# Kernel optimization log

Hardware: AMD Instinct MI355X
Metric: run time of the kernel (lower is better)

The kernel has to match this reference:

```python
import jax, jax.numpy as jnp
import numpy as np
from jax import lax

B, BERT_DIM, Z_DIM, ODE_UNITS, T_MAX = 4096, 768, 64, 128, 512
LN_EPS = 1e-5

def _glorot(key, shape):
    fan_in, fan_out = shape[0], shape[1]
    lim = float(np.sqrt(6.0 / (fan_in + fan_out)))
    return jax.random.uniform(key, shape, jnp.float32, -lim, lim)

def setup_inputs() -> dict:
    key = jax.random.key(0)
    ks = jax.random.split(key, 16)
    inp = {
        'bert_emb': jax.random.normal(ks[0], (B, BERT_DIM), jnp.float32),
        'times': jax.random.uniform(ks[1], (B, T_MAX), jnp.float32),
        'seq_lens': jax.random.randint(ks[2], (B,), 0, T_MAX).astype(jnp.int64),
        'eps': jax.random.normal(ks[3], (B, Z_DIM), jnp.float32),
        # bert_proj: Linear(768->64) + LayerNorm(64)
        'proj_W': _glorot(ks[4], (BERT_DIM, Z_DIM)),
        'proj_b': jnp.zeros((Z_DIM,), jnp.float32),
        'ln_g': jnp.ones((Z_DIM,), jnp.float32),
        'ln_b': jnp.zeros((Z_DIM,), jnp.float32),
        # DiffusionAug
        'log_noise_std': jnp.float32(-2.0),
        'den_W1': _glorot(ks[5], (Z_DIM, 2 * Z_DIM)),
        'den_b1': jnp.zeros((2 * Z_DIM,), jnp.float32),
        'den_W2': _glorot(ks[6], (2 * Z_DIM, Z_DIM)),
        'den_b2': jnp.zeros((Z_DIM,), jnp.float32),
        # ODEFunc: Linear->Tanh->Linear->Tanh->Linear (xavier_uniform, zero bias)
        'ode_W1': _glorot(ks[7], (Z_DIM, ODE_UNITS)),
        'ode_b1': jnp.zeros((ODE_UNITS,), jnp.float32),
        'ode_W2': _glorot(ks[8], (ODE_UNITS, ODE_UNITS)),
        'ode_b2': jnp.zeros((ODE_UNITS,), jnp.float32),
        'ode_W3': _glorot(ks[9], (ODE_UNITS, Z_DIM)),
        'ode_b3': jnp.zeros((Z_DIM,), jnp.float32),
        # dec_head: Linear(64->2)
        'dec_W': _glorot(ks[10], (Z_DIM, 2)),
        'dec_b': jnp.zeros((2,), jnp.float32),
    }
    return inp

def reference(bert_emb, times, seq_lens, eps, proj_W, proj_b, ln_g, ln_b,
              log_noise_std, den_W1, den_b1, den_W2, den_b2,
              ode_W1, ode_b1, ode_W2, ode_b2, ode_W3, ode_b3, dec_W, dec_b):
    T = times.shape[1]
    # bert_proj: Linear + LayerNorm (dropout = identity in eval)
    h = bert_emb @ proj_W + proj_b
    mu = jnp.mean(h, axis=-1, keepdims=True)
    var = jnp.var(h, axis=-1, keepdims=True)
    z_clean = (h - mu) * lax.rsqrt(var + LN_EPS) * ln_g + ln_b
    # DiffusionAug: noise + denoise MLP, MSE to detached clean latent
    sigma = jax.nn.softplus(log_noise_std)
    z_noisy = z_clean + sigma * eps
    z_aug = jax.nn.silu(z_noisy @ den_W1 + den_b1) @ den_W2 + den_b2
    diff_loss = jnp.mean((z_aug - lax.stop_gradient(z_clean)) ** 2)
    # Euler ODE integration: z <- z + dt * f(z), T sequential steps
    dt = jnp.float32(1.0 / max(T, 1))
    def step(z, _):
        f = jnp.tanh(jnp.tanh(z @ ode_W1 + ode_b1) @ ode_W2 + ode_b2) @ ode_W3 + ode_b3
        z_new = z + dt * f
        return z_new, z_new
    _, zs = lax.scan(step, z_aug, None, length=T)  # zs: (T, B, z)
    traj = jnp.concatenate([z_aug[:, None, :], jnp.swapaxes(zs, 0, 1)], axis=1)  # (B, T+1, z)
    out = traj @ dec_W + dec_b  # (B, T+1, 2)
    pred_delta = out[:, :, 0]
    stop_logits = out[:, :, 1]
    return (pred_delta, stop_logits, diff_loss)
```

## Files before the change

kernel.cpp:

```cpp
#include <hip/hip_runtime.h>
#include <stdint.h>

#define NB 4096
#define NT 512
#define OT 513
#define TOTE (NB*OT)
#define LOSSOFF (2*TOTE)

typedef float  f32x4 __attribute__((ext_vector_type(4)));
typedef __fp16 f16x8 __attribute__((ext_vector_type(8)));
typedef __fp16 f16x2 __attribute__((ext_vector_type(2)));

#define MFMA(A,B,C) __builtin_amdgcn_mfma_f32_16x16x32_f16((A),(B),(C),0,0,0)

__device__ __forceinline__ void wg_barrier() {
  asm volatile("s_waitcnt lgkmcnt(0)\n\ts_barrier" ::: "memory");
}

__device__ __forceinline__ float fast_tanh(float x) {
  float e = __builtin_amdgcn_exp2f(x * 2.8853900817779268f);
  return __builtin_fmaf(-2.0f, __builtin_amdgcn_rcpf(1.0f + e), 1.0f);
}
__device__ __forceinline__ f32x4 tanh4(f32x4 x) {
  f32x4 m = x * 2.8853900817779268f;
  f32x4 e;
  e.x = __builtin_amdgcn_exp2f(m.x); e.y = __builtin_amdgcn_exp2f(m.y);
  e.z = __builtin_amdgcn_exp2f(m.z); e.w = __builtin_amdgcn_exp2f(m.w);
  f32x4 o = e + 1.0f;
  f32x4 r;
  r.x = __builtin_amdgcn_rcpf(o.x); r.y = __builtin_amdgcn_rcpf(o.y);
  r.z = __builtin_amdgcn_rcpf(o.z); r.w = __builtin_amdgcn_rcpf(o.w);
  return __builtin_elementwise_fma((f32x4)(-2.0f), r, (f32x4)(1.0f));
}
__device__ __forceinline__ float fast_silu(float x) {
  float e = __builtin_amdgcn_exp2f(x * -1.4426950408889634f);
  return x * __builtin_amdgcn_rcpf(1.0f + e);
}
__device__ __forceinline__ uint32_t pk2(float a, float b) {
  union { f16x2 h; uint32_t u; } c;
  c.h = __builtin_amdgcn_cvt_pkrtz(a, b);
  return c.u;
}
__device__ __forceinline__ f16x8 pack8(f32x4 a, f32x4 b) {
  union { f16x8 v; f16x2 h[4]; } u;
  u.h[0] = __builtin_amdgcn_cvt_pkrtz(a.x, a.y);
  u.h[1] = __builtin_amdgcn_cvt_pkrtz(a.z, a.w);
  u.h[2] = __builtin_amdgcn_cvt_pkrtz(b.x, b.y);
  u.h[3] = __builtin_amdgcn_cvt_pkrtz(b.z, b.w);
  return u.v;
}

#define WS_WPAK (1u<<20)
#define WS_UBUF ((1u<<20) + (256u<<10))
#define WS_CBUF ((1u<<20) + (384u<<10))

__global__ void compose_kernel(const float* __restrict__ oW1, const float* __restrict__ oW3,
                               const float* __restrict__ ob3, const float* __restrict__ dW,
                               float* __restrict__ Ubuf, float* __restrict__ cbuf,
                               float* __restrict__ dout) {
  int g = blockIdx.x, tid = threadIdx.x;
  if (g < 72) {
    int e = g * 256 + tid;
    int i = e / 144, j = e - i * 144;
    float s = 0.f;
    if (j < 128) {
      #pragma unroll 4
      for (int k = 0; k < 64; k++) s = __builtin_fmaf(oW3[i * 64 + k], oW1[k * 128 + j], s);
    } else if (j < 130) {
      int cc = j - 128;
      for (int k = 0; k < 64; k++) s = __builtin_fmaf(oW3[i * 64 + k], dW[k * 2 + cc], s);
    }
    Ubuf[i * 144 + j] = s;
  } else {
    if (tid < 144) {
      float s = 0.f;
      if (tid < 128) {
        for (int k = 0; k < 64; k++) s = __builtin_fmaf(ob3[k], oW1[k * 128 + tid], s);
      } else if (tid < 130) {
        int cc = tid - 128;
        for (int k = 0; k < 64; k++) s = __builtin_fmaf(ob3[k], dW[k * 2 + cc], s);
      }
      cbuf[tid] = s;
    }
    if (tid == 255) dout[LOSSOFF] = 0.0f;
  }
}

__global__ void pack_kernel(const float* __restrict__ oW1, const float* __restrict__ oW2,
                            const float* __restrict__ dW,  const float* __restrict__ dW1,
                            const float* __restrict__ dW2, const float* __restrict__ pW,
                            const float* __restrict__ Ubuf, char* __restrict__ wdst) {
  int g = blockIdx.x * 256 + threadIdx.x;
  int fid = g >> 6, lane = g & 63;
  if (fid >= 228 || (fid >= 50 && fid < 64)) return;
  int m4 = lane & 15;
  if (fid >= 48 && fid < 50) {
    int kt = fid - 48;
    int k0 = kt * 32 + (lane >> 4) * 8;
    f16x8 out;
    #pragma unroll
    for (int j = 0; j < 8; j++) out[j] = (m4 < 2) ? (__fp16)dW[(k0 + j) * 2 + m4] : (__fp16)0.f;
    *(f16x8*)(wdst + (size_t)(fid * 64 + lane) * 16) = out;
    return;
  }
  const float* src; int Kt, M, base;
  if      (fid < 16)  { src = oW1;  Kt = 2;  M = 128; base = 0;   }
  else if (fid < 48)  { src = oW2;  Kt = 4;  M = 128; base = 16;  }
  else if (fid < 80)  { src = dW1;  Kt = 2;  M = 128; base = 64;  }
  else if (fid < 96)  { src = dW2;  Kt = 4;  M = 64;  base = 80;  }
  else if (fid < 192) { src = pW;   Kt = 24; M = 64;  base = 96;  }
  else                { src = Ubuf; Kt = 4;  M = 144; base = 192; }
  int local = fid - base;
  int mt = local / Kt, kt = local % Kt;
  int m  = mt * 16 + m4;
  int k0 = kt * 32 + (lane >> 4) * 8;
  f16x8 out;
  #pragma unroll
  for (int j = 0; j < 8; j++) out[j] = (__fp16)src[(size_t)(k0 + j) * M + m];
  *(f16x8*)(wdst + (size_t)(fid * 64 + lane) * 16) = out;
}

__global__ __launch_bounds__(512, 2) void prologue_kernel(
    const float* __restrict__ bert, const float* __restrict__ eps,
    const float* __restrict__ projb, const float* __restrict__ lng,
    const float* __restrict__ lnb,  const float* __restrict__ lns,
    const float* __restrict__ db1,  const float* __restrict__ db2,
    const char* __restrict__ wpack, float* __restrict__ wsz,
    float* __restrict__ dout) {
  __shared__ __attribute__((aligned(16))) char sZ[16 * 128];
  __shared__ __attribute__((aligned(16))) char sH[16 * 256];
  __shared__ f32x4  sScr[4 * 64];
  __shared__ float2 sMV[64];
  __shared__ float  sLsum[4];

  const int tid  = threadIdx.x;
  const int wave = tid >> 6, lane = tid & 63;
  const int q = lane >> 4, b = lane & 15;
  const int bg = blockIdx.x * 16 + b;
  const int b7 = b & 7;
  const f16x8* wp = (const f16x8*)wpack;
  const int u0 = wave * 16 + q * 4;

  const int zr0 = b * 128 + ((q    ) ^ b7) * 16;
  const int zr1 = b * 128 + ((q + 4) ^ b7) * 16;
  int hr[4];
  #pragma unroll
  for (int s = 0; s < 4; s++) hr[s] = b * 256 + ((4 * s + q) ^ b7) * 16;
  const int hw = b * 256 + (((2 * wave + (q >> 1)) ^ b7) * 16) + (q & 1) * 8;
  const int zw = b * 128 + (((2 * (wave & 3) + (q >> 1)) ^ b7) * 16) + (q & 1) * 8;

  const int mt = wave & 3, kh = wave >> 2;
  f32x4 hA = {0,0,0,0}, hB = {0,0,0,0};
  #pragma unroll 4
  for (int i = 0; i < 12; i++) {
    int kt = kh * 12 + i;
    f16x8 af = wp[(size_t)(96 + mt * 24 + kt) * 64 + lane];
    const float* bp = bert + (size_t)bg * 768 + kt * 32 + q * 8;
    f32x4 f0 = *(const f32x4*)bp;
    f32x4 f1 = *(const f32x4*)(bp + 4);
    f16x8 bf = pack8(f0, f1);
    if (i & 1) hB = MFMA(af, bf, hB); else hA = MFMA(af, bf, hA);
  }
  f32x4 hacc = hA + hB;
  if (wave >= 4) sScr[(wave - 4) * 64 + lane] = hacc;
  __syncthreads();

  f32x4 h = {0,0,0,0}, zc = {0,0,0,0};
  if (wave < 4) {
    h = hacc + sScr[wave * 64 + lane];
    h.x += projb[u0 + 0]; h.y += projb[u0 + 1];
    h.z += projb[u0 + 2]; h.w += projb[u0 + 3];
    float s1 = h.x + h.y + h.z + h.w;
    float s2 = h.x*h.x + h.y*h.y + h.z*h.z + h.w*h.w;
    s1 += __shfl_xor(s1, 16); s1 += __shfl_xor(s1, 32);
    s2 += __shfl_xor(s2, 16); s2 += __shfl_xor(s2, 32);
    if (q == 0) sMV[wave * 16 + b] = make_float2(s1, s2);
  }
  __syncthreads();
  if (wave < 4) {
    float t1 = 0.f, t2 = 0.f;
    #pragma unroll
    for (int w2 = 0; w2 < 4; w2++) { float2 m = sMV[w2 * 16 + b]; t1 += m.x; t2 += m.y; }
    float mu  = t1 * (1.0f / 64.0f);
    float var = t2 * (1.0f / 64.0f) - mu * mu;
    float rs  = rsqrtf(var + 1e-5f);
    float sigma = logf(1.0f + expf(lns[0]));
    f32x4 e = *(const f32x4*)(eps + (size_t)bg * 64 + u0);
    zc.x = __builtin_fmaf((h.x - mu) * rs, lng[u0+0], lnb[u0+0]);
    zc.y = __builtin_fmaf((h.y - mu) * rs, lng[u0+1], lnb[u0+1]);
    zc.z = __builtin_fmaf((h.z - mu) * rs, lng[u0+2], lnb[u0+2]);
    zc.w = __builtin_fmaf((h.w - mu) * rs, lng[u0+3], lnb[u0+3]);
    f32x4 zn = zc + sigma * e;
    *(uint2*)(sZ + zw) = make_uint2(pk2(zn.x, zn.y), pk2(zn.z, zn.w));
  }
  __syncthreads();
  {
    f16x8 w0 = wp[(size_t)(64 + wave * 2 + 0) * 64 + lane];
    f16x8 w1 = wp[(size_t)(64 + wave * 2 + 1) * 64 + lane];
    f16x8 bz0 = *(const f16x8*)(sZ + zr0);
    f16x8 bz1 = *(const f16x8*)(sZ + zr1);
    f32x4 bias = { db1[u0+0], db1[u0+1], db1[u0+2], db1[u0+3] };
    f32x4 acc = MFMA(w0, bz0, bias);
    acc = MFMA(w1, bz1, acc);
    *(uint2*)(sH + hw) = make_uint2(pk2(fast_silu(acc.x), fast_silu(acc.y)),
                                    pk2(fast_silu(acc.z), fast_silu(acc.w)));
  }
  __syncthreads();
  if (wave < 4) {
    f16x8 w0 = wp[(size_t)(80 + wave * 4 + 0) * 64 + lane];
    f16x8 w1 = wp[(size_t)(80 + wave * 4 + 1) * 64 + lane];
    f16x8 w2 = wp[(size_t)(80 + wave * 4 + 2) * 64 + lane];
    f16x8 w3 = wp[(size_t)(80 + wave * 4 + 3) * 64 + lane];
    f16x8 g0 = *(const f16x8*)(sH + hr[0]);
    f16x8 g1 = *(const f16x8*)(sH + hr[1]);
    f16x8 g2 = *(const f16x8*)(sH + hr[2]);
    f16x8 g3 = *(const f16x8*)(sH + hr[3]);
    f32x4 bias = { db2[u0+0], db2[u0+1], db2[u0+2], db2[u0+3] };
    const f32x4 z4 = {0,0,0,0};
    f32x4 aA = MFMA(w0, g0, bias); aA = MFMA(w1, g1, aA);
    f32x4 aB = MFMA(w2, g2, z4);   aB = MFMA(w3, g3, aB);
    f32x4 za = aA + aB;
    *(f32x4*)(wsz + (size_t)bg * 64 + u0) = za;
    f32x4 d = za - zc;
    float sl = d.x*d.x + d.y*d.y + d.z*d.z + d.w*d.w;
    const int offs[6] = {1, 2, 4, 8, 16, 32};
    #pragma unroll
    for (int i = 0; i < 6; i++) sl += __shfl_xor(sl, offs[i]);
    if (lane == 0) sLsum[wave] = sl;
  }
  __syncthreads();
  if (tid == 0)
    atomicAdd(dout + LOSSOFF,
              (sLsum[0] + sLsum[1] + sLsum[2] + sLsum[3]) * (1.0f / 262144.0f));
}

__global__ __launch_bounds__(512, 1) void ode_kernel(
    const float* __restrict__ wsz, const char* __restrict__ wpack,
    const float* __restrict__ ob1, const float* __restrict__ cbuf,
    const float* __restrict__ ob2, const float* __restrict__ decb,
    float* __restrict__ dout) {
  __shared__ __attribute__((aligned(16))) char sH1[4096];
  __shared__ __attribute__((aligned(16))) char sH2[4096];

  const int tid  = threadIdx.x;
  const int wave = tid >> 6, lane = tid & 63;
  const int q = lane >> 4, b = lane & 15;
  const f16x8* wp = (const f16x8*)wpack;
  const float dtc = 1.0f / 512.0f;
  const f32x4 dt4 = {dtc, dtc, dtc, dtc};
  const f32x4 zero4 = {0,0,0,0};

  int rd[4];
  #pragma unroll
  for (int kt = 0; kt < 4; kt++) rd[kt] = b * 256 + (((kt * 4 + q) ^ b) * 16);
  const int wr = b * 256 + (((wave * 2 + (q >> 1)) ^ b) * 16) + (q & 1) * 8;

  f16x8 w2f[4], uf[4], uf8[4];
  #pragma unroll
  for (int kt = 0; kt < 4; kt++) {
    w2f[kt] = wp[(size_t)(16  + wave * 4 + kt) * 64 + lane];
    uf [kt] = wp[(size_t)(192 + wave * 4 + kt) * 64 + lane];
  }
  const bool dec = (wave == 7);
  if (dec) {
    #pragma unroll
    for (int kt = 0; kt < 4; kt++)
      uf8[kt] = wp[(size_t)(192 + 32 + kt) * 64 + lane];
  }
  const f32x4 b2f = *(const f32x4*)(ob2  + wave * 16 + q * 4);
  const f32x4 cw  = *(const f32x4*)(cbuf + wave * 16 + q * 4);
  const f32x4 c8  = *(const f32x4*)(cbuf + 128 + q * 4);

  const int bg = blockIdx.x * 16 + b;
  const float* zrow = wsz + (size_t)bg * 64;
  f32x4 z0a = *(const f32x4*)(zrow + q * 8);
  f32x4 z0b = *(const f32x4*)(zrow + q * 8 + 4);
  f32x4 z1a = *(const f32x4*)(zrow + 32 + q * 8);
  f32x4 z1b = *(const f32x4*)(zrow + 32 + q * 8 + 4);
  f16x8 zf0 = pack8(z0a, z0b);
  f16x8 zf1 = pack8(z1a, z1b);

  f32x4 b1v = *(const f32x4*)(ob1 + wave * 16 + q * 4);
  f32x4 G = MFMA(wp[(size_t)(wave * 2 + 0) * 64 + lane], zf0, b1v);
  G = MFMA(wp[(size_t)(wave * 2 + 1) * 64 + lane], zf1, G);
  {
    f32x4 th = tanh4(G);
    *(uint2*)(sH1 + wr) = make_uint2(pk2(th.x, th.y), pk2(th.z, th.w));
  }

  f32x4 Gd = zero4;
  float* const outp_p = dout + (size_t)bg * OT;
  float* const outp_s = dout + (size_t)TOTE + (size_t)bg * OT;
  if (dec) {
    f32x4 b1d = zero4;
    if (q == 0) { b1d.x = decb[0]; b1d.y = decb[1]; }
    Gd = MFMA(wp[(size_t)48 * 64 + lane], zf0, b1d);
    Gd = MFMA(wp[(size_t)49 * 64 + lane], zf1, Gd);
    if (q == 0) { outp_p[0] = Gd.x; outp_s[0] = Gd.y; }
  }
  wg_barrier();

  #define PHASE_A() do {                                                     \
    f16x8 p0 = *(const f16x8*)(sH1 + rd[0]);                                 \
    f16x8 p1 = *(const f16x8*)(sH1 + rd[1]);                                 \
    f16x8 p2 = *(const f16x8*)(sH1 + rd[2]);                                 \
    f16x8 p3 = *(const f16x8*)(sH1 + rd[3]);                                 \
    f32x4 a  = MFMA(w2f[0], p0, b2f);                                        \
    a  = MFMA(w2f[1], p1, a);                                                \
    f32x4 a2 = MFMA(w2f[2], p2, zero4);                                      \
    a2 = MFMA(w2f[3], p3, a2);                                               \
    f32x4 th = tanh4(a + a2);                                                \
    *(uint2*)(sH2 + wr) = make_uint2(pk2(th.x, th.y), pk2(th.z, th.w));      \
  } while (0)

  #define PHASE_B_UPD(Ra,Rb,Rc,Rd_) do {                                     \
    f32x4 d  = MFMA(uf[0], Ra, cw);                                          \
    d  = MFMA(uf[1], Rb, d);                                                 \
    f32x4 d2 = MFMA(uf[2], Rc, zero4);                                       \
    d2 = MFMA(uf[3], Rd_, d2);                                               \
    G = __builtin_elementwise_fma(dt4, d + d2, G);                           \
    f32x4 th = tanh4(G);                                                     \
    *(uint2*)(sH1 + wr) = make_uint2(pk2(th.x, th.y), pk2(th.z, th.w));      \
  } while (0)

  #define DECODE(Ra,Rb,Rc,Rd_) do {                                         \
    f32x4 e  = MFMA(uf8[0], Ra, c8);                                         \
    e  = MFMA(uf8[1], Rb, e);                                                \
    f32x4 e2 = MFMA(uf8[2], Rc, zero4);                                      \
    e2 = MFMA(uf8[3], Rd_, e2);                                              \
    Gd = __builtin_elementwise_fma(dt4, e + e2, Gd);                         \
  } while (0)

  f16x8 X0, X1, X2, X3, Y0, Y1, Y2, Y3;
  #pragma unroll 1
  for (int t = 0; t < NT; t += 2) {
    PHASE_A();
    wg_barrier();
    X0 = *(const f16x8*)(sH2 + rd[0]);
    X1 = *(const f16x8*)(sH2 + rd[1]);
    X2 = *(const f16x8*)(sH2 + rd[2]);
    X3 = *(const f16x8*)(sH2 + rd[3]);
    if (dec && t > 0) {
      DECODE(Y0, Y1, Y2, Y3);
      if (q == 0) { outp_p[t] = Gd.x; outp_s[t] = Gd.y; }
    }
    PHASE_B_UPD(X0, X1, X2, X3);
    wg_barrier();

    PHASE_A();
    wg_barrier();
    Y0 = *(const f16x8*)(sH2 + rd[0]);
    Y1 = *(const f16x8*)(sH2 + rd[1]);
    Y2 = *(const f16x8*)(sH2 + rd[2]);
    Y3 = *(const f16x8*)(sH2 + rd[3]);
    if (dec) {
      DECODE(X0, X1, X2, X3);
      if (q == 0) { outp_p[t + 1] = Gd.x; outp_s[t + 1] = Gd.y; }
    }
    PHASE_B_UPD(Y0, Y1, Y2, Y3);
    wg_barrier();
  }
  if (dec) {
    DECODE(Y0, Y1, Y2, Y3);
    if (q == 0) { outp_p[NT] = Gd.x; outp_s[NT] = Gd.y; }
  }
  #undef PHASE_A
  #undef PHASE_B_UPD
  #undef DECODE
}

extern "C" void kernel_launch(void* const* d_in, const int* in_sizes, int n_in,
                              void* d_out, int out_size, void* d_ws, size_t ws_size,
                              hipStream_t stream) {
  const float* bert  = (const float*)d_in[0];
  const float* eps   = (const float*)d_in[3];
  const float* projW = (const float*)d_in[4];
  const float* projb = (const float*)d_in[5];
  const float* lng   = (const float*)d_in[6];
  const float* lnb   = (const float*)d_in[7];
  const float* lns   = (const float*)d_in[8];
  const float* denW1 = (const float*)d_in[9];
  const float* denb1 = (const float*)d_in[10];
  const float* denW2 = (const float*)d_in[11];
  const float* denb2 = (const float*)d_in[12];
  const float* odeW1 = (const float*)d_in[13];
  const float* odeb1 = (const float*)d_in[14];
  const float* odeW2 = (const float*)d_in[15];
  const float* odeb2 = (const float*)d_in[16];
  const float* odeW3 = (const float*)d_in[17];
  const float* odeb3 = (const float*)d_in[18];
  const float* decW  = (const float*)d_in[19];
  const float* decb  = (const float*)d_in[20];
  float* dout = (float*)d_out;

  float* wsz  = (float*)d_ws;
  char*  wpak = (char*)d_ws + WS_WPAK;
  float* Ubuf = (float*)((char*)d_ws + WS_UBUF);
  float* cbuf = (float*)((char*)d_ws + WS_CBUF);

  compose_kernel<<<73, 256, 0, stream>>>(odeW1, odeW3, odeb3, decW, Ubuf, cbuf, dout);
  pack_kernel<<<57, 256, 0, stream>>>(odeW1, odeW2, decW, denW1, denW2, projW, Ubuf, wpak);
  prologue_kernel<<<256, 512, 0, stream>>>(bert, eps, projb, lng, lnb, lns,
                                           denb1, denb2, wpak, wsz, dout);
  ode_kernel<<<256, 512, 0, stream>>>(wsz, wpak, odeb1, cbuf, odeb2, decb, dout);
}
```

Baseline: 410.3 us.

## Split ODE kernel into 512 blocks of 4 waves, 8 batch rows each

The ODE kernel now runs 512 workgroups of 256 threads, each handling 8 batch rows instead of 16, with each wave computing two 16-unit output tiles. The 16-column MFMA has its upper 8 columns duplicated, and only lanes with b<8 write. The aim is to spread the work over all compute units and get shorter, cheaper barriers across 4 waves with two independent MFMA chains per wave. In exchange, half of the MFMA throughput is spent on redundant columns, and each wave does twice the serial work per step.

```diff
diff --git a/kernel.cpp b/kernel.cpp
--- a/kernel.cpp
+++ b/kernel.cpp
@@ -234,17 +234,19 @@
               (sLsum[0] + sLsum[1] + sLsum[2] + sLsum[3]) * (1.0f / 262144.0f));
 }
 
-__global__ __launch_bounds__(512, 1) void ode_kernel(
+__global__ __launch_bounds__(256, 2) void ode_kernel(
     const float* __restrict__ wsz, const char* __restrict__ wpack,
     const float* __restrict__ ob1, const float* __restrict__ cbuf,
     const float* __restrict__ ob2, const float* __restrict__ decb,
     float* __restrict__ dout) {
-  __shared__ __attribute__((aligned(16))) char sH1[4096];
-  __shared__ __attribute__((aligned(16))) char sH2[4096];
+  __shared__ __attribute__((aligned(16))) char sH1[2048];
+  __shared__ __attribute__((aligned(16))) char sH2[2048];
 
   const int tid  = threadIdx.x;
   const int wave = tid >> 6, lane = tid & 63;
   const int q = lane >> 4, b = lane & 15;
+  const int br = b & 7;
+  const bool rw = (b < 8);
   const f16x8* wp = (const f16x8*)wpack;
   const float dtc = 1.0f / 512.0f;
   const f32x4 dt4 = {dtc, dtc, dtc, dtc};
@@ -252,26 +254,40 @@
 
   int rd[4];
   #pragma unroll
-  for (int kt = 0; kt < 4; kt++) rd[kt] = b * 256 + (((kt * 4 + q) ^ b) * 16);
-  const int wr = b * 256 + (((wave * 2 + (q >> 1)) ^ b) * 16) + (q & 1) * 8;
-
-  f16x8 w2f[4], uf[4], uf8[4];
-  #pragma unroll
-  for (int kt = 0; kt < 4; kt++) {
-    w2f[kt] = wp[(size_t)(16  + wave * 4 + kt) * 64 + lane];
-    uf [kt] = wp[(size_t)(192 + wave * 4 + kt) * 64 + lane];
-  }
-  const bool dec = (wave == 7);
+  for (int kt = 0; kt < 4; kt++) rd[kt] = br * 256 + (((kt * 4 + q) ^ br) * 16);
+  int wr[2];
+  #pragma unroll
+  for (int s = 0; s < 2; s++) {
+    int T = wave + 4 * s;
+    wr[s] = br * 256 + (((T * 2 + (q >> 1)) ^ br) * 16) + (q & 1) * 8;
+  }
+
+  f16x8 w2f[2][4], uf[2][4], uf8[4];
+  #pragma unroll
+  for (int s = 0; s < 2; s++) {
+    int T = wave + 4 * s;
+    #pragma unroll
+    for (int kt = 0; kt < 4; kt++) {
+      w2f[s][kt] = wp[(size_t)(16  + T * 4 + kt) * 64 + lane];
+      uf [s][kt] = wp[(size_t)(192 + T * 4 + kt) * 64 + lane];
+    }
+  }
+  const bool dec = (wave == 3);
   if (dec) {
     #pragma unroll
     for (int kt = 0; kt < 4; kt++)
       uf8[kt] = wp[(size_t)(192 + 32 + kt) * 64 + lane];
   }
-  const f32x4 b2f = *(const f32x4*)(ob2  + wave * 16 + q * 4);
-  const f32x4 cw  = *(const f32x4*)(cbuf + wave * 16 + q * 4);
-  const f32x4 c8  = *(const f32x4*)(cbuf + 128 + q * 4);
-
-  const int bg = blockIdx.x * 16 + b;
+  f32x4 b2f[2], cw[2];
+  #pragma unroll
+  for (int s = 0; s < 2; s++) {
+    int T = wave + 4 * s;
+    b2f[s] = *(const f32x4*)(ob2  + T * 16 + q * 4);
+    cw [s] = *(const f32x4*)(cbuf + T * 16 + q * 4);
+  }
+  const f32x4 c8 = *(const f32x4*)(cbuf + 128 + q * 4);
+
+  const int bg = blockIdx.x * 8 + br;
   const float* zrow = wsz + (size_t)bg * 64;
   f32x4 z0a = *(const f32x4*)(zrow + q * 8);
   f32x4 z0b = *(const f32x4*)(zrow + q * 8 + 4);
@@ -280,12 +296,15 @@
   f16x8 zf0 = pack8(z0a, z0b);
   f16x8 zf1 = pack8(z1a, z1b);
 
-  f32x4 b1v = *(const f32x4*)(ob1 + wave * 16 + q * 4);
-  f32x4 G = MFMA(wp[(size_t)(wave * 2 + 0) * 64 + lane], zf0, b1v);
-  G = MFMA(wp[(size_t)(wave * 2 + 1) * 64 + lane], zf1, G);
-  {
-    f32x4 th = tanh4(G);
-    *(uint2*)(sH1 + wr) = make_uint2(pk2(th.x, th.y), pk2(th.z, th.w));
+  f32x4 G[2];
+  #pragma unroll
+  for (int s = 0; s < 2; s++) {
+    int T = wave + 4 * s;
+    f32x4 b1v = *(const f32x4*)(ob1 + T * 16 + q * 4);
+    G[s] = MFMA(wp[(size_t)(T * 2 + 0) * 64 + lane], zf0, b1v);
+    G[s] = MFMA(wp[(size_t)(T * 2 + 1) * 64 + lane], zf1, G[s]);
+    f32x4 th = tanh4(G[s]);
+    if (rw) *(uint2*)(sH1 + wr[s]) = make_uint2(pk2(th.x, th.y), pk2(th.z, th.w));
   }
 
   f32x4 Gd = zero4;
@@ -296,7 +315,7 @@
     if (q == 0) { b1d.x = decb[0]; b1d.y = decb[1]; }
     Gd = MFMA(wp[(size_t)48 * 64 + lane], zf0, b1d);
     Gd = MFMA(wp[(size_t)49 * 64 + lane], zf1, Gd);
-    if (q == 0) { outp_p[0] = Gd.x; outp_s[0] = Gd.y; }
+    if (q == 0 && rw) { outp_p[0] = Gd.x; outp_s[0] = Gd.y; }
   }
   wg_barrier();
 
@@ -305,22 +324,39 @@
     f16x8 p1 = *(const f16x8*)(sH1 + rd[1]);                                 \
     f16x8 p2 = *(const f16x8*)(sH1 + rd[2]);                                 \
     f16x8 p3 = *(const f16x8*)(sH1 + rd[3]);                                 \
-    f32x4 a  = MFMA(w2f[0], p0, b2f);                                        \
-    a  = MFMA(w2f[1], p1, a);                                                \
-    f32x4 a2 = MFMA(w2f[2], p2, zero4);                                      \
-    a2 = MFMA(w2f[3], p3, a2);                                               \
-    f32x4 th = tanh4(a + a2);                                                \
-    *(uint2*)(sH2 + wr) = make_uint2(pk2(th.x, th.y), pk2(th.z, th.w));      \
+    f32x4 A0 = MFMA(w2f[0][0], p0, b2f[0]);                                  \
+    f32x4 A1 = MFMA(w2f[1][0], p0, b2f[1]);                                  \
+    A0 = MFMA(w2f[0][1], p1, A0);                                            \
+    A1 = MFMA(w2f[1][1], p1, A1);                                            \
+    f32x4 B0 = MFMA(w2f[0][2], p2, zero4);                                   \
+    f32x4 B1 = MFMA(w2f[1][2], p2, zero4);                                   \
+    B0 = MFMA(w2f[0][3], p3, B0);                                            \
+    B1 = MFMA(w2f[1][3], p3, B1);                                            \
+    f32x4 t0 = tanh4(A0 + B0);                                               \
+    f32x4 t1 = tanh4(A1 + B1);                                               \
+    if (rw) {                                                                \
+      *(uint2*)(sH2 + wr[0]) = make_uint2(pk2(t0.x, t0.y), pk2(t0.z, t0.w)); \
+      *(uint2*)(sH2 + wr[1]) = make_uint2(pk2(t1.x, t1.y), pk2(t1.z, t1.w)); \
+    }                                                                        \
   } while (0)
 
   #define PHASE_B_UPD(Ra,Rb,Rc,Rd_) do {                                     \
-    f32x4 d  = MFMA(uf[0], Ra, cw);                                          \
-    d  = MFMA(uf[1], Rb, d);                                                 \
-    f32x4 d2 = MFMA(uf[2], Rc, zero4);                                       \
-    d2 = MFMA(uf[3], Rd_, d2);                                               \
-    G = __builtin_elementwise_fma(dt4, d + d2, G);                           \
-    f32x4 th = tanh4(G);                                                     \
-    *(uint2*)(sH1 + wr) = make_uint2(pk2(th.x, th.y), pk2(th.z, th.w));      \
+    f32x4 D0 = MFMA(uf[0][0], Ra, cw[0]);                                    \
+    f32x4 D1 = MFMA(uf[1][0], Ra, cw[1]);                                    \
+    D0 = MFMA(uf[0][1], Rb, D0);                                             \
+    D1 = MFMA(uf[1][1], Rb, D1);                                             \
+    f32x4 E0 = MFMA(uf[0][2], Rc, zero4);                                    \
+    f32x4 E1 = MFMA(uf[1][2], Rc, zero4);                                    \
+    E0 = MFMA(uf[0][3], Rd_, E0);                                            \
+    E1 = MFMA(uf[1][3], Rd_, E1);                                            \
+    G[0] = __builtin_elementwise_fma(dt4, D0 + E0, G[0]);                    \
+    G[1] = __builtin_elementwise_fma(dt4, D1 + E1, G[1]);                    \
+    f32x4 t0 = tanh4(G[0]);                                                  \
+    f32x4 t1 = tanh4(G[1]);                                                  \
+    if (rw) {                                                                \
+      *(uint2*)(sH1 + wr[0]) = make_uint2(pk2(t0.x, t0.y), pk2(t0.z, t0.w)); \
+      *(uint2*)(sH1 + wr[1]) = make_uint2(pk2(t1.x, t1.y), pk2(t1.z, t1.w)); \
+    }                                                                        \
   } while (0)
 
   #define DECODE(Ra,Rb,Rc,Rd_) do {                                         \
@@ -328,7 +364,8 @@
     e  = MFMA(uf8[1], Rb, e);                                                \
     f32x4 e2 = MFMA(uf8[2], Rc, zero4);                                      \
     e2 = MFMA(uf8[3], Rd_, e2);                                              \
-    Gd = __builtin_elementwise_fma(dt4, e + e2, Gd);                         \
+    Gd.x = __builtin_fmaf(dtc, e.x + e2.x, Gd.x);                            \
+    Gd.y = __builtin_fmaf(dtc, e.y + e2.y, Gd.y);                            \
   } while (0)
 
   f16x8 X0, X1, X2, X3, Y0, Y1, Y2, Y3;
@@ -342,7 +379,7 @@
     X3 = *(const f16x8*)(sH2 + rd[3]);
     if (dec && t > 0) {
       DECODE(Y0, Y1, Y2, Y3);
-      if (q == 0) { outp_p[t] = Gd.x; outp_s[t] = Gd.y; }
+      if (q == 0 && rw) { outp_p[t] = Gd.x; outp_s[t] = Gd.y; }
     }
     PHASE_B_UPD(X0, X1, X2, X3);
     wg_barrier();
@@ -355,14 +392,14 @@
     Y3 = *(const f16x8*)(sH2 + rd[3]);
     if (dec) {
       DECODE(X0, X1, X2, X3);
-      if (q == 0) { outp_p[t + 1] = Gd.x; outp_s[t + 1] = Gd.y; }
+      if (q == 0 && rw) { outp_p[t + 1] = Gd.x; outp_s[t + 1] = Gd.y; }
     }
     PHASE_B_UPD(Y0, Y1, Y2, Y3);
     wg_barrier();
   }
   if (dec) {
     DECODE(Y0, Y1, Y2, Y3);
-    if (q == 0) { outp_p[NT] = Gd.x; outp_s[NT] = Gd.y; }
+    if (q == 0 && rw) { outp_p[NT] = Gd.x; outp_s[NT] = Gd.y; }
   }
   #undef PHASE_A
   #undef PHASE_B_UPD
@@ -402,5 +439,5 @@
   pack_kernel<<<57, 256, 0, stream>>>(odeW1, odeW2, decW, denW1, denW2, projW, Ubuf, wpak);
   prologue_kernel<<<256, 512, 0, stream>>>(bert, eps, projb, lng, lnb, lns,
                                            denb1, denb2, wpak, wsz, dout);
-  ode_kernel<<<256, 512, 0, stream>>>(wsz, wpak, odeb1, cbuf, odeb2, decb, dout);
-}
+  ode_kernel<<<512, 256, 0, stream>>>(wsz, wpak, odeb1, cbuf, odeb2, decb, dout);
+}
```

Measured after the change: 556.4 us. 35.6% more time.

## Fuse weight-compose into pack kernel and defer decode MFMA results across barrier

Applied to the files above, without the earlier changes.

Merges compose_kernel into pack_kernel: the composed W3·W1 / W3·decW weights are now computed directly inside the packing threads, and the bias-composition and loss zeroing move to an extra block, which removes one launch and the Ubuf round trip. In the ODE loop, the decode MFMAs are issued after the state update and their results are consumed one half-step later, so the MFMA latency is hidden behind the barrier. The decode lanes also raise wave priority via s_setprio. Each packing thread now does redundant 64-long dot products, and more registers stay live across the barrier.

```diff
diff --git a/kernel.cpp b/kernel.cpp
--- a/kernel.cpp
+++ b/kernel.cpp
@@ -17,10 +17,6 @@
   asm volatile("s_waitcnt lgkmcnt(0)\n\ts_barrier" ::: "memory");
 }
 
-__device__ __forceinline__ float fast_tanh(float x) {
-  float e = __builtin_amdgcn_exp2f(x * 2.8853900817779268f);
-  return __builtin_fmaf(-2.0f, __builtin_amdgcn_rcpf(1.0f + e), 1.0f);
-}
 __device__ __forceinline__ f32x4 tanh4(f32x4 x) {
   f32x4 m = x * 2.8853900817779268f;
   f32x4 e;
@@ -51,27 +47,18 @@
 }
 
 #define WS_WPAK (1u<<20)
-#define WS_UBUF ((1u<<20) + (256u<<10))
 #define WS_CBUF ((1u<<20) + (384u<<10))
 
-__global__ void compose_kernel(const float* __restrict__ oW1, const float* __restrict__ oW3,
-                               const float* __restrict__ ob3, const float* __restrict__ dW,
-                               float* __restrict__ Ubuf, float* __restrict__ cbuf,
-                               float* __restrict__ dout) {
-  int g = blockIdx.x, tid = threadIdx.x;
-  if (g < 72) {
-    int e = g * 256 + tid;
-    int i = e / 144, j = e - i * 144;
-    float s = 0.f;
-    if (j < 128) {
-      #pragma unroll 4
-      for (int k = 0; k < 64; k++) s = __builtin_fmaf(oW3[i * 64 + k], oW1[k * 128 + j], s);
-    } else if (j < 130) {
-      int cc = j - 128;
-      for (int k = 0; k < 64; k++) s = __builtin_fmaf(oW3[i * 64 + k], dW[k * 2 + cc], s);
-    }
-    Ubuf[i * 144 + j] = s;
-  } else {
+__global__ void pack_kernel(const float* __restrict__ oW1, const float* __restrict__ oW2,
+                            const float* __restrict__ dW,  const float* __restrict__ dW1,
+                            const float* __restrict__ dW2, const float* __restrict__ pW,
+                            const float* __restrict__ oW3, const float* __restrict__ ob3,
+                            float* __restrict__ cbuf, char* __restrict__ wdst,
+                            float* __restrict__ dout) {
+  int g = blockIdx.x * 256 + threadIdx.x;
+  int fid = g >> 6, lane = g & 63;
+  if (fid >= 228) {
+    int tid = g - 228 * 64;
     if (tid < 144) {
       float s = 0.f;
       if (tid < 128) {
@@ -83,16 +70,9 @@
       cbuf[tid] = s;
     }
     if (tid == 255) dout[LOSSOFF] = 0.0f;
-  }
-}
-
-__global__ void pack_kernel(const float* __restrict__ oW1, const float* __restrict__ oW2,
-                            const float* __restrict__ dW,  const float* __restrict__ dW1,
-                            const float* __restrict__ dW2, const float* __restrict__ pW,
-                            const float* __restrict__ Ubuf, char* __restrict__ wdst) {
-  int g = blockIdx.x * 256 + threadIdx.x;
-  int fid = g >> 6, lane = g & 63;
-  if (fid >= 228 || (fid >= 50 && fid < 64)) return;
+    return;
+  }
+  if (fid >= 50 && fid < 64) return;
   int m4 = lane & 15;
   if (fid >= 48 && fid < 50) {
     int kt = fid - 48;
@@ -103,13 +83,32 @@
     *(f16x8*)(wdst + (size_t)(fid * 64 + lane) * 16) = out;
     return;
   }
+  if (fid >= 192) {
+    int local = fid - 192, mt = local >> 2, kt = local & 3;
+    int m  = mt * 16 + m4;
+    int k0 = kt * 32 + (lane >> 4) * 8;
+    f16x8 out;
+    #pragma unroll
+    for (int j = 0; j < 8; j++) {
+      float s = 0.f;
+      const float* w3r = oW3 + (size_t)(k0 + j) * 64;
+      if (m < 128) {
+        for (int k = 0; k < 64; k++) s = __builtin_fmaf(w3r[k], oW1[k * 128 + m], s);
+      } else if (m < 130) {
+        int cc = m - 128;
+        for (int k = 0; k < 64; k++) s = __builtin_fmaf(w3r[k], dW[k * 2 + cc], s);
+      }
+      out[j] = (__fp16)s;
+    }
+    *(f16x8*)(wdst + (size_t)(fid * 64 + lane) * 16) = out;
+    return;
+  }
   const float* src; int Kt, M, base;
   if      (fid < 16)  { src = oW1;  Kt = 2;  M = 128; base = 0;   }
   else if (fid < 48)  { src = oW2;  Kt = 4;  M = 128; base = 16;  }
   else if (fid < 80)  { src = dW1;  Kt = 2;  M = 128; base = 64;  }
   else if (fid < 96)  { src = dW2;  Kt = 4;  M = 64;  base = 80;  }
-  else if (fid < 192) { src = pW;   Kt = 24; M = 64;  base = 96;  }
-  else                { src = Ubuf; Kt = 4;  M = 144; base = 192; }
+  else                { src = pW;   Kt = 24; M = 64;  base = 96;  }
   int local = fid - base;
   int mt = local / Kt, kt = local % Kt;
   int m  = mt * 16 + m4;
@@ -289,6 +288,7 @@
   }
 
   f32x4 Gd = zero4;
+  f32x4 eA = zero4, eB = zero4;
   float* const outp_p = dout + (size_t)bg * OT;
   float* const outp_s = dout + (size_t)TOTE + (size_t)bg * OT;
   if (dec) {
@@ -323,12 +323,17 @@
     *(uint2*)(sH1 + wr) = make_uint2(pk2(th.x, th.y), pk2(th.z, th.w));      \
   } while (0)
 
-  #define DECODE(Ra,Rb,Rc,Rd_) do {                                         \
-    f32x4 e  = MFMA(uf8[0], Ra, c8);                                         \
-    e  = MFMA(uf8[1], Rb, e);                                                \
-    f32x4 e2 = MFMA(uf8[2], Rc, zero4);                                      \
-    e2 = MFMA(uf8[3], Rd_, e2);                                              \
-    Gd = __builtin_elementwise_fma(dt4, e + e2, Gd);                         \
+  #define DEC_ISSUE(Ra,Rb,Rc,Rd_) do {                                      \
+    eA = MFMA(uf8[0], Ra, c8);                                               \
+    eA = MFMA(uf8[1], Rb, eA);                                               \
+    eB = MFMA(uf8[2], Rc, zero4);                                            \
+    eB = MFMA(uf8[3], Rd_, eB);                                              \
+  } while (0)
+
+  #define DEC_CONSUME(ti) do {                                              \
+    Gd.x = __builtin_fmaf(dtc, eA.x + eB.x, Gd.x);                           \
+    Gd.y = __builtin_fmaf(dtc, eA.y + eB.y, Gd.y);                           \
+    if (q == 0) { outp_p[ti] = Gd.x; outp_s[ti] = Gd.y; }                    \
   } while (0)
 
   f16x8 X0, X1, X2, X3, Y0, Y1, Y2, Y3;
@@ -340,11 +345,15 @@
     X1 = *(const f16x8*)(sH2 + rd[1]);
     X2 = *(const f16x8*)(sH2 + rd[2]);
     X3 = *(const f16x8*)(sH2 + rd[3]);
-    if (dec && t > 0) {
-      DECODE(Y0, Y1, Y2, Y3);
-      if (q == 0) { outp_p[t] = Gd.x; outp_s[t] = Gd.y; }
+    if (dec) {
+      __builtin_amdgcn_s_setprio(1);
+      if (t > 0) DEC_CONSUME(t);
     }
     PHASE_B_UPD(X0, X1, X2, X3);
+    if (dec) {
+      DEC_ISSUE(X0, X1, X2, X3);
+      __builtin_amdgcn_s_setprio(0);
+    }
     wg_barrier();
 
     PHASE_A();
@@ -354,19 +363,21 @@
     Y2 = *(const f16x8*)(sH2 + rd[2]);
     Y3 = *(const f16x8*)(sH2 + rd[3]);
     if (dec) {
-      DECODE(X0, X1, X2, X3);
-      if (q == 0) { outp_p[t + 1] = Gd.x; outp_s[t + 1] = Gd.y; }
+      __builtin_amdgcn_s_setprio(1);
+      DEC_CONSUME(t + 1);
     }
     PHASE_B_UPD(Y0, Y1, Y2, Y3);
+    if (dec) {
+      DEC_ISSUE(Y0, Y1, Y2, Y3);
+      __builtin_amdgcn_s_setprio(0);
+    }
     wg_barrier();
   }
-  if (dec) {
-    DECODE(Y0, Y1, Y2, Y3);
-    if (q == 0) { outp_p[NT] = Gd.x; outp_s[NT] = Gd.y; }
-  }
+  if (dec) DEC_CONSUME(NT);
   #undef PHASE_A
   #undef PHASE_B_UPD
-  #undef DECODE
+  #undef DEC_ISSUE
+  #undef DEC_CONSUME
 }
 
 extern "C" void kernel_launch(void* const* d_in, const int* in_sizes, int n_in,
@@ -395,11 +406,10 @@
 
   float* wsz  = (float*)d_ws;
   char*  wpak = (char*)d_ws + WS_WPAK;
-  float* Ubuf = (float*)((char*)d_ws + WS_UBUF);
   float* cbuf = (float*)((char*)d_ws + WS_CBUF);
 
-  compose_kernel<<<73, 256, 0, stream>>>(odeW1, odeW3, odeb3, decW, Ubuf, cbuf, dout);
-  pack_kernel<<<57, 256, 0, stream>>>(odeW1, odeW2, decW, denW1, denW2, projW, Ubuf, wpak);
+  pack_kernel<<<58, 256, 0, stream>>>(odeW1, odeW2, decW, denW1, denW2, projW,
+                                      odeW3, odeb3, cbuf, wpak, dout);
   prologue_kernel<<<256, 512, 0, stream>>>(bert, eps, projb, lng, lnb, lns,
                                            denb1, denb2, wpak, wsz, dout);
   ode_kernel<<<256, 512, 0, stream>>>(wsz, wpak, odeb1, cbuf, odeb2, decb, dout);
```

Result: faster. 400.9 us (-2.3%).
